# Performance work log

Measured on AMD Instinct MI355X. Metric: run time of the kernel, lower is better.

The kernel has to match this reference:

```python
import jax, jax.numpy as jnp
import numpy as np

TOP_K = 2
NEG_INF = -1e30


def setup_inputs() -> dict:
    key = jax.random.key(0)
    ks = jax.random.split(key, 9)
    S, B, D, H, E, O = 2, 2048, 1024, 2048, 8, 1024
    return {
        "xs": jax.random.normal(ks[0], (S, B, D), jnp.float32),
        "Wg": jax.random.normal(ks[1], (D, E), jnp.float32),
        "b": jax.random.normal(ks[2], (E,), jnp.float32),
        "fc1_w": jax.random.normal(ks[3], (E, H, D), jnp.float32) * 0.02,
        "fc1_b": jax.random.normal(ks[4], (E, H), jnp.float32) * 0.02,
        "fc2_w": jax.random.normal(ks[5], (E, H, H), jnp.float32) * 0.02,
        "fc2_b": jax.random.normal(ks[6], (E, H), jnp.float32) * 0.02,
        "final_w": jax.random.normal(ks[7], (O, H), jnp.float32) * 0.02,
        "final_b": jax.random.normal(ks[8], (O,), jnp.float32) * 0.02,
    }


def reference(xs, Wg, b, fc1_w, fc1_b, fc2_w, fc2_b, final_w, final_b):
    # xs: [S, B, D] stacked x_list
    S = xs.shape[0]
    # gate logits H: [S, B, E]
    Hg = jnp.einsum('sbd,de->sbe', xs, Wg) + b
    expert_probs = jax.nn.softmax(Hg, axis=-1)  # per-view full softmax
    # top-k threshold mask (H >= kth largest value)
    topk_vals = jax.lax.top_k(Hg, TOP_K)[0]          # [S, B, K]
    thr = topk_vals[..., -1:]                         # [S, B, 1]
    H_masked = jnp.where(Hg >= thr, Hg, NEG_INF)
    G = jax.nn.softmax(H_masked, axis=-1)             # [S, B, E]
    # dense all-expert FFN: [S, B, E, H]
    h = jnp.einsum('sbd,ehd->sbeh', xs, fc1_w) + fc1_b
    h = jax.nn.relu(h)
    eo = jnp.einsum('sbeh,egh->sbeg', h, fc2_w) + fc2_b
    # gated sum over experts, averaged over views: [B, H]
    combined = jnp.einsum('sbe,sbeh->bh', G, eo) / S
    out = combined @ final_w.T + final_b               # [B, O]
    return out, expert_probs
```

## Files before the change

### kernel.cpp

```cpp
#include <hip/hip_runtime.h>
#include <stdint.h>

#define S_DIM 2
#define B_DIM 2048
#define D_DIM 1024
#define H_DIM 2048
#define E_DIM 8
#define O_DIM 1024
#define NTOK 4096
#define CAP 12288

typedef __attribute__((ext_vector_type(8))) short bf16x8;
typedef __attribute__((ext_vector_type(4))) float f32x4;

__device__ __forceinline__ unsigned short f2bf(float f) {
    union { float f; uint32_t i; } c; c.f = f;
    uint32_t r = c.i + 0x7FFFu + ((c.i >> 16) & 1u);
    return (unsigned short)(r >> 16);
}
__device__ __forceinline__ uint32_t pack2(float a, float b) {
    return (uint32_t)f2bf(a) | ((uint32_t)f2bf(b) << 16);
}
__device__ __forceinline__ void stage8(const float* __restrict__ src,
                                       unsigned short* __restrict__ dst) {
    float4 f0 = *(const float4*)src;
    float4 f1 = *(const float4*)(src + 4);
    int4 v;
    v.x = (int)pack2(f0.x, f0.y);
    v.y = (int)pack2(f0.z, f0.w);
    v.z = (int)pack2(f1.x, f1.y);
    v.w = (int)pack2(f1.z, f1.w);
    *(int4*)dst = v;
}

__global__ __launch_bounds__(256) void gating_kernel(
    const float* __restrict__ xs,
    const float* __restrict__ Wg,
    const float* __restrict__ bvec,
    float* __restrict__ probs_out,
    int* __restrict__ counts,
    int* __restrict__ sel_cnt,
    int* __restrict__ sel_e,
    float* __restrict__ sel_g)
{
    const int wave = threadIdx.x >> 6;
    const int lane = threadIdx.x & 63;
    const int t = blockIdx.x * 4 + wave;
    const float* x = xs + (size_t)t * D_DIM;

    float acc[8];
#pragma unroll
    for (int e = 0; e < 8; ++e) acc[e] = 0.f;

#pragma unroll
    for (int i = 0; i < D_DIM / 64; ++i) {
        int d = i * 64 + lane;
        float xv = x[d];
        float4 w0 = *(const float4*)(Wg + (size_t)d * 8);
        float4 w1 = *(const float4*)(Wg + (size_t)d * 8 + 4);
        acc[0] += xv * w0.x; acc[1] += xv * w0.y;
        acc[2] += xv * w0.z; acc[3] += xv * w0.w;
        acc[4] += xv * w1.x; acc[5] += xv * w1.y;
        acc[6] += xv * w1.z; acc[7] += xv * w1.w;
    }
#pragma unroll
    for (int off = 32; off > 0; off >>= 1) {
#pragma unroll
        for (int e = 0; e < 8; ++e)
            acc[e] += __shfl_down(acc[e], off);
    }

    if (lane == 0) {
        float Hg[8];
#pragma unroll
        for (int e = 0; e < 8; ++e) Hg[e] = acc[e] + bvec[e];

        int a1 = 0;
#pragma unroll
        for (int e = 1; e < 8; ++e) if (Hg[e] > Hg[a1]) a1 = e;
        float m1 = Hg[a1];
        float m2 = -1e30f;
#pragma unroll
        for (int e = 0; e < 8; ++e) if (e != a1 && Hg[e] > m2) m2 = Hg[e];

        float ex[8]; float sum = 0.f;
#pragma unroll
        for (int e = 0; e < 8; ++e) { ex[e] = expf(Hg[e] - m1); sum += ex[e]; }
        float inv = 1.f / sum;
#pragma unroll
        for (int e = 0; e < 8; ++e)
            probs_out[(size_t)t * 8 + e] = ex[e] * inv;

        float den = 0.f;
#pragma unroll
        for (int e = 0; e < 8; ++e) if (Hg[e] >= m2) den += ex[e];
        float invd = 1.f / den;
        int n = 0;
#pragma unroll
        for (int e = 0; e < 8; ++e) {
            if (Hg[e] >= m2) {
                sel_e[t * 8 + n] = e;
                sel_g[t * 8 + n] = ex[e] * invd;
                ++n;
                atomicAdd(&counts[e], 1);
            }
        }
        sel_cnt[t] = n;
    }
}

__global__ void scan_kernel(const int* __restrict__ counts, int* __restrict__ offsets)
{
    if (threadIdx.x == 0) {
        int tot = 0;
#pragma unroll
        for (int e = 0; e < 8; ++e) { offsets[e] = tot; tot += counts[e]; }
    }
}

__global__ __launch_bounds__(256) void scatter_kernel(
    const int* __restrict__ sel_cnt,
    const int* __restrict__ sel_e,
    const float* __restrict__ sel_g,
    const int* __restrict__ offsets,
    int* __restrict__ cursors,
    int* __restrict__ pair_token,
    float* __restrict__ pair_gate)
{
    int t = blockIdx.x * blockDim.x + threadIdx.x;
    if (t >= NTOK) return;
    int n = sel_cnt[t];
    for (int i = 0; i < n && i < 8; ++i) {
        int e = sel_e[t * 8 + i];
        int r = atomicAdd(&cursors[e], 1);
        int slot = offsets[e] + r;
        if (slot < CAP) {
            pair_token[slot] = t;
            pair_gate[slot]  = sel_g[t * 8 + i];
        }
    }
}

__global__ __launch_bounds__(256) void fc1_kernel(
    const float* __restrict__ xs,
    const float* __restrict__ fc1_w,
    const float* __restrict__ fc1_b,
    const int* __restrict__ counts,
    const int* __restrict__ offsets,
    const int* __restrict__ pair_token,
    unsigned short* __restrict__ h)
{
    const int e = blockIdx.z;
    const int cnt = counts[e];
    const int mtile = blockIdx.y;
    if (mtile * 128 >= cnt) return;
    const int ntile = blockIdx.x;
    const int offs = offsets[e];

    __shared__ unsigned short As[128 * 40];
    __shared__ unsigned short Bs[128 * 40];

    const int tid  = threadIdx.x;
    const int lane = tid & 63;
    const int wave = tid >> 6;
    const int wr = wave >> 1, wc = wave & 1;
    const int lrow = lane & 15;
    const int kq   = lane >> 4;
    const int koff = kq * 8;

    const float* aSrc[2];
    const float* bSrc[2];
    int ldsOff[2];
#pragma unroll
    for (int i = 0; i < 2; ++i) {
        int c = tid + i * 256;
        int row = c >> 2;
        int kc  = (c & 3) * 8;
        ldsOff[i] = row * 40 + kc;
        int m = mtile * 128 + row;
        int mc = m < cnt ? m : cnt - 1;
        int tok = pair_token[offs + mc];
        aSrc[i] = xs + (size_t)tok * D_DIM + kc;
        int n = ntile * 128 + row;
        bSrc[i] = fc1_w + ((size_t)e * H_DIM + n) * D_DIM + kc;
    }

    f32x4 acc[4][4];
#pragma unroll
    for (int i = 0; i < 4; ++i)
#pragma unroll
        for (int j = 0; j < 4; ++j)
            acc[i][j] = (f32x4){0.f, 0.f, 0.f, 0.f};

    for (int k0 = 0; k0 < D_DIM; k0 += 32) {
        __syncthreads();
#pragma unroll
        for (int i = 0; i < 2; ++i) {
            stage8(aSrc[i] + k0, &As[ldsOff[i]]);
            stage8(bSrc[i] + k0, &Bs[ldsOff[i]]);
        }
        __syncthreads();
        bf16x8 af[4], bfr[4];
#pragma unroll
        for (int i = 0; i < 4; ++i)
            af[i] = *(const bf16x8*)&As[(wr * 64 + i * 16 + lrow) * 40 + koff];
#pragma unroll
        for (int j = 0; j < 4; ++j)
            bfr[j] = *(const bf16x8*)&Bs[(wc * 64 + j * 16 + lrow) * 40 + koff];
#pragma unroll
        for (int i = 0; i < 4; ++i)
#pragma unroll
            for (int j = 0; j < 4; ++j)
                acc[i][j] = __builtin_amdgcn_mfma_f32_16x16x32_bf16(af[i], bfr[j], acc[i][j], 0, 0, 0);
    }

    int ncol[4]; float bias[4];
#pragma unroll
    for (int j = 0; j < 4; ++j) {
        ncol[j] = ntile * 128 + wc * 64 + j * 16 + lrow;
        bias[j] = fc1_b[e * H_DIM + ncol[j]];
    }
#pragma unroll
    for (int i = 0; i < 4; ++i) {
#pragma unroll
        for (int r = 0; r < 4; ++r) {
            int m = mtile * 128 + wr * 64 + i * 16 + kq * 4 + r;
            if (m < cnt) {
                size_t base = (size_t)(offs + m) * H_DIM;
#pragma unroll
                for (int j = 0; j < 4; ++j) {
                    float v = acc[i][j][r] + bias[j];
                    h[base + ncol[j]] = f2bf(v > 0.f ? v : 0.f);
                }
            }
        }
    }
}

__global__ __launch_bounds__(256) void fc2_kernel(
    const unsigned short* __restrict__ h,
    const float* __restrict__ fc2_w,
    const float* __restrict__ fc2_b,
    const int* __restrict__ counts,
    const int* __restrict__ offsets,
    const int* __restrict__ pair_token,
    const float* __restrict__ pair_gate,
    float* __restrict__ combined)
{
    const int e = blockIdx.z;
    const int cnt = counts[e];
    const int mtile = blockIdx.y;
    if (mtile * 128 >= cnt) return;
    const int ntile = blockIdx.x;
    const int offs = offsets[e];

    __shared__ unsigned short As[128 * 40];
    __shared__ unsigned short Bs[128 * 40];

    const int tid  = threadIdx.x;
    const int lane = tid & 63;
    const int wave = tid >> 6;
    const int wr = wave >> 1, wc = wave & 1;
    const int lrow = lane & 15;
    const int kq   = lane >> 4;
    const int koff = kq * 8;

    const unsigned short* aSrc[2];
    const float* bSrc[2];
    int ldsOff[2];
#pragma unroll
    for (int i = 0; i < 2; ++i) {
        int c = tid + i * 256;
        int row = c >> 2;
        int kc  = (c & 3) * 8;
        ldsOff[i] = row * 40 + kc;
        int m = mtile * 128 + row;
        int mc = m < cnt ? m : cnt - 1;
        aSrc[i] = h + (size_t)(offs + mc) * H_DIM + kc;
        int n = ntile * 128 + row;
        bSrc[i] = fc2_w + ((size_t)e * H_DIM + n) * H_DIM + kc;
    }

    f32x4 acc[4][4];
#pragma unroll
    for (int i = 0; i < 4; ++i)
#pragma unroll
        for (int j = 0; j < 4; ++j)
            acc[i][j] = (f32x4){0.f, 0.f, 0.f, 0.f};

    for (int k0 = 0; k0 < H_DIM; k0 += 32) {
        __syncthreads();
#pragma unroll
        for (int i = 0; i < 2; ++i) {
            *(int4*)&As[ldsOff[i]] = *(const int4*)(aSrc[i] + k0);
            stage8(bSrc[i] + k0, &Bs[ldsOff[i]]);
        }
        __syncthreads();
        bf16x8 af[4], bfr[4];
#pragma unroll
        for (int i = 0; i < 4; ++i)
            af[i] = *(const bf16x8*)&As[(wr * 64 + i * 16 + lrow) * 40 + koff];
#pragma unroll
        for (int j = 0; j < 4; ++j)
            bfr[j] = *(const bf16x8*)&Bs[(wc * 64 + j * 16 + lrow) * 40 + koff];
#pragma unroll
        for (int i = 0; i < 4; ++i)
#pragma unroll
            for (int j = 0; j < 4; ++j)
                acc[i][j] = __builtin_amdgcn_mfma_f32_16x16x32_bf16(af[i], bfr[j], acc[i][j], 0, 0, 0);
    }

    int ncol[4]; float bias[4];
#pragma unroll
    for (int j = 0; j < 4; ++j) {
        ncol[j] = ntile * 128 + wc * 64 + j * 16 + lrow;
        bias[j] = fc2_b[e * H_DIM + ncol[j]];
    }
#pragma unroll
    for (int i = 0; i < 4; ++i) {
#pragma unroll
        for (int r = 0; r < 4; ++r) {
            int m = mtile * 128 + wr * 64 + i * 16 + kq * 4 + r;
            if (m < cnt) {
                int slot = offs + m;
                int tok  = pair_token[slot];
                float g  = pair_gate[slot] * 0.5f;
                int brow = tok & (B_DIM - 1);
#pragma unroll
                for (int j = 0; j < 4; ++j) {
                    float v = (acc[i][j][r] + bias[j]) * g;
                    atomicAdd(&combined[(size_t)brow * H_DIM + ncol[j]], v);
                }
            }
        }
    }
}

__global__ __launch_bounds__(256) void final_kernel(
    const float* __restrict__ combined,
    const float* __restrict__ final_w,
    const float* __restrict__ final_b,
    float* __restrict__ out)
{
    const int mtile = blockIdx.y;
    const int ntile = blockIdx.x;

    __shared__ unsigned short As[128 * 40];
    __shared__ unsigned short Bs[128 * 40];

    const int tid  = threadIdx.x;
    const int lane = tid & 63;
    const int wave = tid >> 6;
    const int wr = wave >> 1, wc = wave & 1;
    const int lrow = lane & 15;
    const int kq   = lane >> 4;
    const int koff = kq * 8;

    const float* aSrc[2];
    const float* bSrc[2];
    int ldsOff[2];
#pragma unroll
    for (int i = 0; i < 2; ++i) {
        int c = tid + i * 256;
        int row = c >> 2;
        int kc  = (c & 3) * 8;
        ldsOff[i] = row * 40 + kc;
        int m = mtile * 128 + row;
        aSrc[i] = combined + (size_t)m * H_DIM + kc;
        int n = ntile * 128 + row;
        bSrc[i] = final_w + (size_t)n * H_DIM + kc;
    }

    f32x4 acc[4][4];
#pragma unroll
    for (int i = 0; i < 4; ++i)
#pragma unroll
        for (int j = 0; j < 4; ++j)
            acc[i][j] = (f32x4){0.f, 0.f, 0.f, 0.f};

    for (int k0 = 0; k0 < H_DIM; k0 += 32) {
        __syncthreads();
#pragma unroll
        for (int i = 0; i < 2; ++i) {
            stage8(aSrc[i] + k0, &As[ldsOff[i]]);
            stage8(bSrc[i] + k0, &Bs[ldsOff[i]]);
        }
        __syncthreads();
        bf16x8 af[4], bfr[4];
#pragma unroll
        for (int i = 0; i < 4; ++i)
            af[i] = *(const bf16x8*)&As[(wr * 64 + i * 16 + lrow) * 40 + koff];
#pragma unroll
        for (int j = 0; j < 4; ++j)
            bfr[j] = *(const bf16x8*)&Bs[(wc * 64 + j * 16 + lrow) * 40 + koff];
#pragma unroll
        for (int i = 0; i < 4; ++i)
#pragma unroll
            for (int j = 0; j < 4; ++j)
                acc[i][j] = __builtin_amdgcn_mfma_f32_16x16x32_bf16(af[i], bfr[j], acc[i][j], 0, 0, 0);
    }

    int ncol[4]; float bias[4];
#pragma unroll
    for (int j = 0; j < 4; ++j) {
        ncol[j] = ntile * 128 + wc * 64 + j * 16 + lrow;
        bias[j] = final_b[ncol[j]];
    }
#pragma unroll
    for (int i = 0; i < 4; ++i) {
#pragma unroll
        for (int r = 0; r < 4; ++r) {
            int m = mtile * 128 + wr * 64 + i * 16 + kq * 4 + r;
#pragma unroll
            for (int j = 0; j < 4; ++j)
                out[(size_t)m * O_DIM + ncol[j]] = acc[i][j][r] + bias[j];
        }
    }
}

extern "C" void kernel_launch(void* const* d_in, const int* in_sizes, int n_in,
                              void* d_out, int out_size, void* d_ws, size_t ws_size,
                              hipStream_t stream) {
    const float* xs      = (const float*)d_in[0];
    const float* Wg      = (const float*)d_in[1];
    const float* bvec    = (const float*)d_in[2];
    const float* fc1_w   = (const float*)d_in[3];
    const float* fc1_b   = (const float*)d_in[4];
    const float* fc2_w   = (const float*)d_in[5];
    const float* fc2_b   = (const float*)d_in[6];
    const float* final_w = (const float*)d_in[7];
    const float* final_b = (const float*)d_in[8];

    float* out = (float*)d_out;
    float* probs_out = out + (size_t)B_DIM * O_DIM;

    uint8_t* w = (uint8_t*)d_ws;
    int*   counts     = (int*)(w + 0);
    int*   cursors    = (int*)(w + 64);
    int*   offsets    = (int*)(w + 128);
    int*   sel_cnt    = (int*)(w + 256);
    int*   sel_e      = (int*)(w + 0x5000);
    float* sel_g      = (float*)(w + 0x25000);
    int*   pair_token = (int*)(w + 0x45000);
    float* pair_gate  = (float*)(w + 0x51000);
    float* combined   = (float*)(w + 0x60000);
    unsigned short* h = (unsigned short*)(w + 0x1060000);

    hipMemsetAsync(w, 0, 256, stream);
    hipMemsetAsync(combined, 0, (size_t)B_DIM * H_DIM * sizeof(float), stream);

    gating_kernel<<<NTOK / 4, 256, 0, stream>>>(xs, Wg, bvec, probs_out,
                                                counts, sel_cnt, sel_e, sel_g);
    scan_kernel<<<1, 64, 0, stream>>>(counts, offsets);
    scatter_kernel<<<NTOK / 256, 256, 0, stream>>>(sel_cnt, sel_e, sel_g, offsets,
                                                   cursors, pair_token, pair_gate);
    fc1_kernel<<<dim3(H_DIM / 128, NTOK / 128, E_DIM), 256, 0, stream>>>(
        xs, fc1_w, fc1_b, counts, offsets, pair_token, h);
    fc2_kernel<<<dim3(H_DIM / 128, NTOK / 128, E_DIM), 256, 0, stream>>>(
        h, fc2_w, fc2_b, counts, offsets, pair_token, pair_gate, combined);
    final_kernel<<<dim3(O_DIM / 128, B_DIM / 128), 256, 0, stream>>>(
        combined, final_w, final_b, out);
}
```

Baseline: 747.1 us.

## Pre-convert weights and activations to bf16 and use direct global-to-LDS loads

Adds conversion kernels that turn fc1/fc2 weights into bf16 buffers each call, and has the gating kernel emit a bf16 copy of xs. The fc1 and fc2 GEMMs then load bf16 tiles straight into LDS with global_load_lds, using an XOR-swizzled 64-wide K tile. This drops the per-tile fp32 load and convert work in the GEMM main loops and halves the bytes the GEMMs read. In exchange, every call pays extra full passes over the weights to convert them and write the bf16 copies.

```diff
diff --git a/kernel.cpp b/kernel.cpp
--- a/kernel.cpp
+++ b/kernel.cpp
@@ -33,6 +33,20 @@
     *(int4*)dst = v;
 }
 
+__device__ __forceinline__ void glds16(const unsigned short* g, unsigned short* l) {
+    __builtin_amdgcn_global_load_lds(
+        (__attribute__((address_space(1))) void*)g,
+        (__attribute__((address_space(3))) void*)l,
+        16, 0, 0);
+}
+
+__global__ __launch_bounds__(256) void convert_kernel(
+    const float* __restrict__ src, unsigned short* __restrict__ dst, int n8)
+{
+    int i = blockIdx.x * blockDim.x + threadIdx.x;
+    if (i < n8) stage8(src + (size_t)i * 8, dst + (size_t)i * 8);
+}
+
 __global__ __launch_bounds__(256) void gating_kernel(
     const float* __restrict__ xs,
     const float* __restrict__ Wg,
@@ -41,7 +55,8 @@
     int* __restrict__ counts,
     int* __restrict__ sel_cnt,
     int* __restrict__ sel_e,
-    float* __restrict__ sel_g)
+    float* __restrict__ sel_g,
+    unsigned short* __restrict__ xs_bf)
 {
     const int wave = threadIdx.x >> 6;
     const int lane = threadIdx.x & 63;
@@ -56,6 +71,7 @@
     for (int i = 0; i < D_DIM / 64; ++i) {
         int d = i * 64 + lane;
         float xv = x[d];
+        xs_bf[(size_t)t * D_DIM + d] = f2bf(xv);
         float4 w0 = *(const float4*)(Wg + (size_t)d * 8);
         float4 w1 = *(const float4*)(Wg + (size_t)d * 8 + 4);
         acc[0] += xv * w0.x; acc[1] += xv * w0.y;
@@ -142,8 +158,8 @@
 }
 
 __global__ __launch_bounds__(256) void fc1_kernel(
-    const float* __restrict__ xs,
-    const float* __restrict__ fc1_w,
+    const unsigned short* __restrict__ xs_bf,
+    const unsigned short* __restrict__ fc1_wb,
     const float* __restrict__ fc1_b,
     const int* __restrict__ counts,
     const int* __restrict__ offsets,
@@ -157,8 +173,8 @@
     const int ntile = blockIdx.x;
     const int offs = offsets[e];
 
-    __shared__ unsigned short As[128 * 40];
-    __shared__ unsigned short Bs[128 * 40];
+    __shared__ __align__(16) unsigned short As[128 * 64];
+    __shared__ __align__(16) unsigned short Bs[128 * 64];
 
     const int tid  = threadIdx.x;
     const int lane = tid & 63;
@@ -166,23 +182,24 @@
     const int wr = wave >> 1, wc = wave & 1;
     const int lrow = lane & 15;
     const int kq   = lane >> 4;
-    const int koff = kq * 8;
-
-    const float* aSrc[2];
-    const float* bSrc[2];
-    int ldsOff[2];
-#pragma unroll
-    for (int i = 0; i < 2; ++i) {
-        int c = tid + i * 256;
-        int row = c >> 2;
-        int kc  = (c & 3) * 8;
-        ldsOff[i] = row * 40 + kc;
+
+    const unsigned short* aSrc[4];
+    const unsigned short* bSrc[4];
+    unsigned short* aDst[4];
+    unsigned short* bDst[4];
+#pragma unroll
+    for (int i = 0; i < 4; ++i) {
+        int c = i * 256 + tid;
+        int row = c >> 3;
+        int gran = (c & 7) ^ (row & 7);
         int m = mtile * 128 + row;
         int mc = m < cnt ? m : cnt - 1;
         int tok = pair_token[offs + mc];
-        aSrc[i] = xs + (size_t)tok * D_DIM + kc;
+        aSrc[i] = xs_bf + (size_t)tok * D_DIM + gran * 8;
         int n = ntile * 128 + row;
-        bSrc[i] = fc1_w + ((size_t)e * H_DIM + n) * D_DIM + kc;
+        bSrc[i] = fc1_wb + ((size_t)e * H_DIM + n) * D_DIM + gran * 8;
+        aDst[i] = &As[(i * 256 + wave * 64) * 8];
+        bDst[i] = &Bs[(i * 256 + wave * 64) * 8];
     }
 
     f32x4 acc[4][4];
@@ -192,26 +209,30 @@
         for (int j = 0; j < 4; ++j)
             acc[i][j] = (f32x4){0.f, 0.f, 0.f, 0.f};
 
-    for (int k0 = 0; k0 < D_DIM; k0 += 32) {
-        __syncthreads();
-#pragma unroll
-        for (int i = 0; i < 2; ++i) {
-            stage8(aSrc[i] + k0, &As[ldsOff[i]]);
-            stage8(bSrc[i] + k0, &Bs[ldsOff[i]]);
-        }
-        __syncthreads();
-        bf16x8 af[4], bfr[4];
-#pragma unroll
-        for (int i = 0; i < 4; ++i)
-            af[i] = *(const bf16x8*)&As[(wr * 64 + i * 16 + lrow) * 40 + koff];
-#pragma unroll
-        for (int j = 0; j < 4; ++j)
-            bfr[j] = *(const bf16x8*)&Bs[(wc * 64 + j * 16 + lrow) * 40 + koff];
-#pragma unroll
-        for (int i = 0; i < 4; ++i)
-#pragma unroll
-            for (int j = 0; j < 4; ++j)
-                acc[i][j] = __builtin_amdgcn_mfma_f32_16x16x32_bf16(af[i], bfr[j], acc[i][j], 0, 0, 0);
+    for (int k0 = 0; k0 < D_DIM; k0 += 64) {
+        __syncthreads();
+#pragma unroll
+        for (int i = 0; i < 4; ++i) {
+            glds16(aSrc[i] + k0, aDst[i]);
+            glds16(bSrc[i] + k0, bDst[i]);
+        }
+        __syncthreads();
+#pragma unroll
+        for (int ks = 0; ks < 2; ++ks) {
+            bf16x8 af[4], bfr[4];
+            const int gr = ks * 4 + kq;
+            const int sg = (gr ^ (lrow & 7)) * 8;
+#pragma unroll
+            for (int i = 0; i < 4; ++i) {
+                af[i]  = *(const bf16x8*)&As[(wr * 64 + i * 16 + lrow) * 64 + sg];
+                bfr[i] = *(const bf16x8*)&Bs[(wc * 64 + i * 16 + lrow) * 64 + sg];
+            }
+#pragma unroll
+            for (int i = 0; i < 4; ++i)
+#pragma unroll
+                for (int j = 0; j < 4; ++j)
+                    acc[i][j] = __builtin_amdgcn_mfma_f32_16x16x32_bf16(af[i], bfr[j], acc[i][j], 0, 0, 0);
+        }
     }
 
     int ncol[4]; float bias[4];
@@ -239,7 +260,7 @@
 
 __global__ __launch_bounds__(256) void fc2_kernel(
     const unsigned short* __restrict__ h,
-    const float* __restrict__ fc2_w,
+    const unsigned short* __restrict__ fc2_wb,
     const float* __restrict__ fc2_b,
     const int* __restrict__ counts,
     const int* __restrict__ offsets,
@@ -254,8 +275,8 @@
     const int ntile = blockIdx.x;
     const int offs = offsets[e];
 
-    __shared__ unsigned short As[128 * 40];
-    __shared__ unsigned short Bs[128 * 40];
+    __shared__ __align__(16) unsigned short As[128 * 64];
+    __shared__ __align__(16) unsigned short Bs[128 * 64];
 
     const int tid  = threadIdx.x;
     const int lane = tid & 63;
@@ -263,22 +284,23 @@
     const int wr = wave >> 1, wc = wave & 1;
     const int lrow = lane & 15;
     const int kq   = lane >> 4;
-    const int koff = kq * 8;
-
-    const unsigned short* aSrc[2];
-    const float* bSrc[2];
-    int ldsOff[2];
-#pragma unroll
-    for (int i = 0; i < 2; ++i) {
-        int c = tid + i * 256;
-        int row = c >> 2;
-        int kc  = (c & 3) * 8;
-        ldsOff[i] = row * 40 + kc;
+
+    const unsigned short* aSrc[4];
+    const unsigned short* bSrc[4];
+    unsigned short* aDst[4];
+    unsigned short* bDst[4];
+#pragma unroll
+    for (int i = 0; i < 4; ++i) {
+        int c = i * 256 + tid;
+        int row = c >> 3;
+        int gran = (c & 7) ^ (row & 7);
         int m = mtile * 128 + row;
         int mc = m < cnt ? m : cnt - 1;
-        aSrc[i] = h + (size_t)(offs + mc) * H_DIM + kc;
+        aSrc[i] = h + (size_t)(offs + mc) * H_DIM + gran * 8;
         int n = ntile * 128 + row;
-        bSrc[i] = fc2_w + ((size_t)e * H_DIM + n) * H_DIM + kc;
+        bSrc[i] = fc2_wb + ((size_t)e * H_DIM + n) * H_DIM + gran * 8;
+        aDst[i] = &As[(i * 256 + wave * 64) * 8];
+        bDst[i] = &Bs[(i * 256 + wave * 64) * 8];
     }
 
     f32x4 acc[4][4];
@@ -288,26 +310,30 @@
         for (int j = 0; j < 4; ++j)
             acc[i][j] = (f32x4){0.f, 0.f, 0.f, 0.f};
 
-    for (int k0 = 0; k0 < H_DIM; k0 += 32) {
-        __syncthreads();
-#pragma unroll
-        for (int i = 0; i < 2; ++i) {
-            *(int4*)&As[ldsOff[i]] = *(const int4*)(aSrc[i] + k0);
-            stage8(bSrc[i] + k0, &Bs[ldsOff[i]]);
-        }
-        __syncthreads();
-        bf16x8 af[4], bfr[4];
-#pragma unroll
-        for (int i = 0; i < 4; ++i)
-            af[i] = *(const bf16x8*)&As[(wr * 64 + i * 16 + lrow) * 40 + koff];
-#pragma unroll
-        for (int j = 0; j < 4; ++j)
-            bfr[j] = *(const bf16x8*)&Bs[(wc * 64 + j * 16 + lrow) * 40 + koff];
-#pragma unroll
-        for (int i = 0; i < 4; ++i)
-#pragma unroll
-            for (int j = 0; j < 4; ++j)
-                acc[i][j] = __builtin_amdgcn_mfma_f32_16x16x32_bf16(af[i], bfr[j], acc[i][j], 0, 0, 0);
+    for (int k0 = 0; k0 < H_DIM; k0 += 64) {
+        __syncthreads();
+#pragma unroll
+        for (int i = 0; i < 4; ++i) {
+            glds16(aSrc[i] + k0, aDst[i]);
+            glds16(bSrc[i] + k0, bDst[i]);
+        }
+        __syncthreads();
+#pragma unroll
+        for (int ks = 0; ks < 2; ++ks) {
+            bf16x8 af[4], bfr[4];
+            const int gr = ks * 4 + kq;
+            const int sg = (gr ^ (lrow & 7)) * 8;
+#pragma unroll
+            for (int i = 0; i < 4; ++i) {
+                af[i]  = *(const bf16x8*)&As[(wr * 64 + i * 16 + lrow) * 64 + sg];
+                bfr[i] = *(const bf16x8*)&Bs[(wc * 64 + i * 16 + lrow) * 64 + sg];
+            }
+#pragma unroll
+            for (int i = 0; i < 4; ++i)
+#pragma unroll
+                for (int j = 0; j < 4; ++j)
+                    acc[i][j] = __builtin_amdgcn_mfma_f32_16x16x32_bf16(af[i], bfr[j], acc[i][j], 0, 0, 0);
+        }
     }
 
     int ncol[4]; float bias[4];
@@ -345,8 +371,8 @@
     const int mtile = blockIdx.y;
     const int ntile = blockIdx.x;
 
-    __shared__ unsigned short As[128 * 40];
-    __shared__ unsigned short Bs[128 * 40];
+    __shared__ __align__(16) unsigned short As[128 * 40];
+    __shared__ __align__(16) unsigned short Bs[128 * 40];
 
     const int tid  = threadIdx.x;
     const int lane = tid & 63;
@@ -445,19 +471,27 @@
     float* pair_gate  = (float*)(w + 0x51000);
     float* combined   = (float*)(w + 0x60000);
     unsigned short* h = (unsigned short*)(w + 0x1060000);
+    unsigned short* xs_bf   = (unsigned short*)(w + 0x4060000);
+    unsigned short* fc1_wb  = (unsigned short*)(w + 0x4860000);
+    unsigned short* fc2_wb  = (unsigned short*)(w + 0x6860000);
 
     hipMemsetAsync(w, 0, 256, stream);
     hipMemsetAsync(combined, 0, (size_t)B_DIM * H_DIM * sizeof(float), stream);
 
+    convert_kernel<<<(E_DIM * H_DIM * D_DIM / 8) / 256, 256, 0, stream>>>(
+        fc1_w, fc1_wb, E_DIM * H_DIM * D_DIM / 8);
+    convert_kernel<<<(E_DIM * H_DIM * H_DIM / 8) / 256, 256, 0, stream>>>(
+        fc2_w, fc2_wb, E_DIM * H_DIM * H_DIM / 8);
+
     gating_kernel<<<NTOK / 4, 256, 0, stream>>>(xs, Wg, bvec, probs_out,
-                                                counts, sel_cnt, sel_e, sel_g);
+                                                counts, sel_cnt, sel_e, sel_g, xs_bf);
     scan_kernel<<<1, 64, 0, stream>>>(counts, offsets);
     scatter_kernel<<<NTOK / 256, 256, 0, stream>>>(sel_cnt, sel_e, sel_g, offsets,
                                                    cursors, pair_token, pair_gate);
     fc1_kernel<<<dim3(H_DIM / 128, NTOK / 128, E_DIM), 256, 0, stream>>>(
-        xs, fc1_w, fc1_b, counts, offsets, pair_token, h);
+        xs_bf, fc1_wb, fc1_b, counts, offsets, pair_token, h);
     fc2_kernel<<<dim3(H_DIM / 128, NTOK / 128, E_DIM), 256, 0, stream>>>(
-        h, fc2_w, fc2_b, counts, offsets, pair_token, pair_gate, combined);
+        h, fc2_wb, fc2_b, counts, offsets, pair_token, pair_gate, combined);
     final_kernel<<<dim3(O_DIM / 128, B_DIM / 128), 256, 0, stream>>>(
         combined, final_w, final_b, out);
 }
```

New measurement: 716.9 us. 1.04x faster.
